# Kernel optimization log

Hardware: AMD Instinct MI355X
Metric: run time of the kernel (lower is better)

Reference implementation:

```python
import jax, jax.numpy as jnp
import numpy as np

EPS = 1e-8  # F.cosine_similarity eps


def _cosine(nb, q):
    # nb: [N1, k, d], q: [N1, d] -> [N1, k]
    dot = jnp.einsum('nkd,nd->nk', nb, q)
    nb_norm = jnp.maximum(jnp.linalg.norm(nb, axis=-1), EPS)
    q_norm = jnp.maximum(jnp.linalg.norm(q, axis=-1), EPS)[:, None]
    return dot / (nb_norm * q_norm)


def setup_inputs() -> dict:
    key = jax.random.key(0)
    k0, k1, k2, k3 = jax.random.split(key, 4)
    N1, N2, D = 2048, 50000, 512
    return {
        'query_emb0': jax.random.normal(k0, (N1, D), dtype=jnp.float32),
        'query_emb1': jax.random.normal(k1, (N1, D), dtype=jnp.float32),
        'cand_emb0': jax.random.normal(k2, (N2, D), dtype=jnp.float32),
        'cand_emb1': jax.random.normal(k3, (N2, D), dtype=jnp.float32),
        'k': 32,
    }


def reference(query_emb0, query_emb1, cand_emb0, cand_emb1, k):
    # --- get_KNN_batch: L2 cdist on the ORIGINAL embeddings only (matches torch) ---
    # ||q - c||^2 = ||q||^2 + ||c||^2 - 2 q.c  (GEMM-based, compute-bound)
    q2 = jnp.sum(query_emb0 * query_emb0, axis=1, keepdims=True)       # [N1,1]
    c2 = jnp.sum(cand_emb0 * cand_emb0, axis=1)[None, :]               # [1,N2]
    d2 = jnp.maximum(q2 + c2 - 2.0 * (query_emb0 @ cand_emb0.T), 0.0)  # [N1,N2]
    dist = jnp.sqrt(d2)
    # topk of -distance == k nearest
    _, top_k_idx = jax.lax.top_k(-dist, k)                             # [N1,k]

    # --- get_neighbor_embeddings: gather both tables ---
    nb0 = cand_emb0[top_k_idx]  # [N1,k,d]
    nb1 = cand_emb1[top_k_idx]  # [N1,k,d]

    # --- compute_cosine_batch: elementwise max of the two cosine tables ---
    cos0 = _cosine(nb0, query_emb0)
    cos1 = _cosine(nb1, query_emb1)
    cosine_table = jnp.where(cos0 > cos1, cos0, cos1)                  # [N1,k]
    return cosine_table, jnp.mean(cosine_table, axis=-1)
```

## Files before the change

kernel.cpp:

```cpp
#include <hip/hip_runtime.h>
#include <math.h>


#define D       512
#define KSEL    32
#define NSELMX  64
#define NCF     8
#define TOPL    5
#define CEPS    1e-8f
#define INF     __builtin_inff()

#define MTF     32
#define NTF     256
#define KCF     64
#define NTHF    256

#define MT      64
#define NT      512
#define KC      64
#define NTH     512

using s16x8  = __attribute__((ext_vector_type(8)))  short;
using f32x16 = __attribute__((ext_vector_type(16))) float;

__device__ __forceinline__ void async16(const void* g, void* s) {
  __builtin_amdgcn_global_load_lds(
      (const __attribute__((address_space(1))) unsigned int*)g,
      (__attribute__((address_space(3))) unsigned int*)s, 16, 0, 0);
}

__device__ __forceinline__ unsigned int bfhi2(float x0, float x1) {
  unsigned int u0 = __float_as_uint(x0), u1 = __float_as_uint(x1);
  u0 = (u0 + 0x7fffu + ((u0 >> 16) & 1u)) >> 16;
  u1 = (u1 + 0x7fffu + ((u1 >> 16) & 1u)) & 0xffff0000u;
  return u0 | u1;
}

__global__ __launch_bounds__(256) void sumsq_cvt_kernel(
    const float* __restrict__ C, const float* __restrict__ Q,
    float* __restrict__ c2, float* __restrict__ q2,
    unsigned short* __restrict__ Cb, unsigned short* __restrict__ Qb,
    int n2, int n1)
{
  int wid  = threadIdx.x >> 6;
  int lane = threadIdx.x & 63;
  int row  = blockIdx.x * 4 + wid;
  const float* src; float* dst; unsigned short* bdst;
  if (row < n2) { src = C + (size_t)row * D; dst = c2 + row; bdst = Cb + (size_t)row * D; }
  else {
    int r = row - n2; if (r >= n1) return;
    src = Q + (size_t)r * D; dst = q2 + r; bdst = Qb + (size_t)r * D;
  }
  const float4* s4 = (const float4*)src;
  float4 a = s4[2*lane], b = s4[2*lane + 1];
  float s = a.x*a.x + a.y*a.y + a.z*a.z + a.w*a.w
          + b.x*b.x + b.y*b.y + b.z*b.z + b.w*b.w;
  int4 h;
  h.x = (int)bfhi2(a.x, a.y); h.y = (int)bfhi2(a.z, a.w);
  h.z = (int)bfhi2(b.x, b.y); h.w = (int)bfhi2(b.z, b.w);
  *(int4*)(bdst + 8*lane) = h;
  #pragma unroll
  for (int o = 32; o > 0; o >>= 1) s += __shfl_down(s, o, 64);
  if (lane == 0) *dst = s;
}

__global__ __launch_bounds__(256) void rows_sumsq_kernel(
    const float* __restrict__ C, const float* __restrict__ Q,
    float* __restrict__ c2, float* __restrict__ q2, int n2, int n1)
{
  int wid  = threadIdx.x >> 6;
  int lane = threadIdx.x & 63;
  int row  = blockIdx.x * 4 + wid;
  const float* src; float* dst;
  if (row < n2) { src = C + (size_t)row * D; dst = c2 + row; }
  else { int r = row - n2; if (r >= n1) return; src = Q + (size_t)r * D; dst = q2 + r; }
  const float4* s4 = (const float4*)src;
  float4 a = s4[lane], b = s4[lane + 64];
  float s = a.x*a.x + a.y*a.y + a.z*a.z + a.w*a.w
          + b.x*b.x + b.y*b.y + b.z*b.z + b.w*b.w;
  #pragma unroll
  for (int o = 32; o > 0; o >>= 1) s += __shfl_down(s, o, 64);
  if (lane == 0) *dst = s;
}

__device__ inline void worst_reduce(float dIn, int iIn, float& wd, int& wi) {
  float dd = dIn; int ii = iIn;
  #pragma unroll
  for (int o = 1; o <= 16; o <<= 1) {
    float dp = __shfl_xor(dd, o, 64);
    int   ip = __shfl_xor(ii, o, 64);
    bool take = (dp > dd) || (dp == dd && ip > ii);
    dd = take ? dp : dd; ii = take ? ip : ii;
  }
  wd = __shfl(dd, 0, 64); wi = __shfl(ii, 0, 64);
}

__device__ inline void cvt8(const float4 a, const float4 b, int4& hi, int4& lo) {
  float x[8] = {a.x, a.y, a.z, a.w, b.x, b.y, b.z, b.w};
  unsigned int hw[8], lw[8];
  #pragma unroll
  for (int j = 0; j < 8; ++j) {
    unsigned int ux = __float_as_uint(x[j]);
    unsigned int rh = (ux + 0x7fffu + ((ux >> 16) & 1u)) & 0xffff0000u;
    float rl = x[j] - __uint_as_float(rh);
    unsigned int ul = __float_as_uint(rl);
    hw[j] = rh >> 16;
    lw[j] = (ul + 0x7fffu + ((ul >> 16) & 1u)) >> 16;
  }
  hi = make_int4((int)(hw[0]|(hw[1]<<16)), (int)(hw[2]|(hw[3]<<16)),
                 (int)(hw[4]|(hw[5]<<16)), (int)(hw[6]|(hw[7]<<16)));
  lo = make_int4((int)(lw[0]|(lw[1]<<16)), (int)(lw[2]|(lw[3]<<16)),
                 (int)(lw[4]|(lw[5]<<16)), (int)(lw[6]|(lw[7]<<16)));
}

__global__ __launch_bounds__(NTHF, 2) void knn_phase1_bf_kernel(
    const unsigned short* __restrict__ Qb, const unsigned short* __restrict__ Cb,
    const float* __restrict__ q2g, const float* __restrict__ c2g,
    float* __restrict__ tkd, int* __restrict__ tki,
    int n1, int n2, int chunk, int nc)
{
  extern __shared__ char smem[];
  unsigned short* qh = (unsigned short*)smem;
  unsigned short* ch = (unsigned short*)(smem + 8192);
  float* dl = (float*)(smem + 73728);

  const int tid  = threadIdx.x;
  const int w    = tid >> 6;
  const int l    = tid & 63;
  const int l31  = l & 31;
  const int half = l >> 5;
  const int bid     = blockIdx.x;
  const int chunkid = bid & (NCF - 1);
  const int mbase   = (bid >> 3) * MTF;
  const int cbase0  = chunkid * chunk;
  const int cend    = min(cbase0 + chunk, n2);

  float q2w[8];
  #pragma unroll
  for (int g = 0; g < 8; ++g)
    q2w[g] = q2g[min(mbase + 8*(g>>1) + 2*w + (g&1), n1 - 1)];

  unsigned long long vv[8][TOPL];
  #pragma unroll
  for (int g = 0; g < 8; ++g)
    #pragma unroll
    for (int t = 0; t < TOPL; ++t) vv[g][t] = 0xffffffffffffffffULL;

  const int lrow = l >> 3;
  const int su   = (l & 7) ^ lrow;

  auto STAGE = [&](int buf, int kb, int cb) {
    {
      int gm = min(mbase + w*8 + lrow, n1 - 1);
      const unsigned short* src = Qb + (size_t)gm * D + kb*KCF + su*8;
      unsigned short* dst = qh + buf*(32*64) + (w*8)*64;
      async16(src, dst);
    }
    #pragma unroll
    for (int i = 0; i < 8; ++i) {
      int gn = cb + w*64 + i*8 + lrow;
      const unsigned short* src = Cb + (size_t)gn * D + kb*KCF + su*8;
      unsigned short* dst = ch + buf*(256*64) + (w*64 + i*8)*64;
      async16(src, dst);
    }
  };

  f32x16 zf;
  #pragma unroll
  for (int e = 0; e < 16; ++e) zf[e] = 0.f;

  const int nsteps = (cend - cbase0 + NTF - 1) / NTF;
  int b = 0;
  STAGE(0, 0, cbase0);
  __syncthreads();

  for (int nt = 0; nt < nsteps; ++nt) {
    const int cbase = cbase0 + nt * NTF;
    f32x16 acc[2];
    acc[0] = zf; acc[1] = zf;

    for (int kb = 0; kb < D/KCF; ++kb) {
      if (kb + 1 < D/KCF) {
        STAGE(b^1, kb+1, cbase);
        asm volatile("s_waitcnt vmcnt(9)" ::: "memory");
      } else if (nt + 1 < nsteps) {
        STAGE(b^1, 0, cbase + NTF);
        asm volatile("s_waitcnt vmcnt(9)" ::: "memory");
      } else {
        asm volatile("s_waitcnt vmcnt(0)" ::: "memory");
      }
      __builtin_amdgcn_s_barrier();
      __builtin_amdgcn_sched_barrier(0);

      const unsigned short* qb  = qh + b*(32*64);
      const unsigned short* cbf = ch + b*(256*64);
      #pragma unroll
      for (int ks = 0; ks < 4; ++ks) {
        const int u = 2*ks + half;
        s16x8 qf, cf[2];
        {
          int r = l31;
          qf = *(const s16x8*)(qb + r*64 + (u ^ (r & 7))*8);
        }
        #pragma unroll
        for (int ct = 0; ct < 2; ++ct) {
          int c = w*64 + ct*32 + l31;
          cf[ct] = *(const s16x8*)(cbf + c*64 + (u ^ (c & 7))*8);
        }
        #pragma unroll
        for (int ct = 0; ct < 2; ++ct)
          acc[ct] = __builtin_amdgcn_mfma_f32_32x32x16_bf16(qf, cf[ct], acc[ct], 0, 0, 0);
      }
      asm volatile("s_waitcnt lgkmcnt(0)" ::: "memory");
      __builtin_amdgcn_s_barrier();
      __builtin_amdgcn_sched_barrier(0);
      b ^= 1;
    }

    float c2v[2]; int vld[2];
    #pragma unroll
    for (int ct = 0; ct < 2; ++ct) {
      int gc = cbase + w*64 + ct*32 + l31;
      vld[ct] = (gc < cend);
      c2v[ct] = vld[ct] ? c2g[gc] : 0.f;
    }
    #pragma unroll
    for (int p = 0; p < 4; ++p) {
      #pragma unroll
      for (int jj = 0; jj < 4; ++jj)
        #pragma unroll
        for (int ct = 0; ct < 2; ++ct) {
          float a = acc[ct][4*p + jj];
          float s = c2v[ct] - 2.f * a;
          dl[(4*half + jj)*NTF + w*64 + ct*32 + l31] = vld[ct] ? s : INF;
        }
      __syncthreads();
      #pragma unroll
      for (int s2 = 0; s2 < 2; ++s2) {
        const int g = 2*p + s2;
        const float q2u = q2w[g];
        #pragma unroll
        for (int j2 = 0; j2 < 4; ++j2) {
          float sv  = dl[(2*w + s2)*NTF + l + 64*j2];
          float d2v = fmaxf(q2u + sv, 0.f);
          unsigned int kbit = __float_as_uint(d2v);
          unsigned int ci = (kbit != 0x7f800000u) ? (unsigned)(cbase + 64*j2 + l)
                                                  : 0x7fffffffu;
          unsigned long long e = ((unsigned long long)kbit << 32) | ci;
          if (e < vv[g][TOPL-1]) {
            vv[g][TOPL-1] = e;
            #pragma unroll
            for (int t = TOPL-1; t > 0; --t) {
              unsigned long long lo = vv[g][t-1] < vv[g][t] ? vv[g][t-1] : vv[g][t];
              unsigned long long hi = vv[g][t-1] < vv[g][t] ? vv[g][t]   : vv[g][t-1];
              vv[g][t-1] = lo; vv[g][t] = hi;
            }
          }
        }
      }
      __syncthreads();
    }
  }

  unsigned long long* sel = (unsigned long long*)smem + (size_t)w * 2048;
  const unsigned long long mlt = (l == 0) ? 0ull : ((~0ull) >> (64 - l));
  __syncthreads();
  #pragma unroll
  for (int g = 0; g < 8; ++g) {
    unsigned int pk = (unsigned int)(vv[g][0] >> 32);
    #pragma unroll
    for (int o = 1; o < 64; o <<= 1) {
      unsigned int other = (unsigned int)__shfl_xor((int)pk, o, 64);
      pk = (other > pk) ? other : pk;
    }
    int cnt = 0;
    #pragma unroll
    for (int t = 0; t < TOPL; ++t) cnt += ((unsigned int)(vv[g][t] >> 32) <= pk) ? 1 : 0;
    unsigned long long b0 = __ballot(cnt & 1);
    unsigned long long b1 = __ballot(cnt & 2);
    unsigned long long b2 = __ballot(cnt & 4);
    int pre = __popcll(b0 & mlt) + 2*__popcll(b1 & mlt) + 4*__popcll(b2 & mlt);
    int Ns  = __popcll(b0) + 2*__popcll(b1) + 4*__popcll(b2);
    #pragma unroll
    for (int t = 0; t < TOPL; ++t)
      if (t < cnt) sel[pre + t] = vv[g][t];
    asm volatile("s_waitcnt lgkmcnt(0)" ::: "memory");
    __builtin_amdgcn_sched_barrier(0);
    int rk[TOPL];
    #pragma unroll
    for (int t = 0; t < TOPL; ++t) rk[t] = 0;
    for (int j = 0; j < Ns; ++j) {
      unsigned long long e = sel[j];
      #pragma unroll
      for (int t = 0; t < TOPL; ++t) rk[t] += (e < vv[g][t]) ? 1 : 0;
    }
    int gq = mbase + 8*(g>>1) + 2*w + (g&1);
    if (gq < n1) {
      #pragma unroll
      for (int t = 0; t < TOPL; ++t)
        if (t < cnt && rk[t] < KSEL) {
          size_t o = ((size_t)gq * nc + chunkid) * KSEL + rk[t];
          tkd[o] = __uint_as_float((unsigned int)(vv[g][t] >> 32));
          tki[o] = (int)(unsigned int)(vv[g][t] & 0xffffffffu);
        }
    }
  }
}

__global__ __launch_bounds__(NTH) void knn_phase1_cvt_kernel(
    const float* __restrict__ Q, const float* __restrict__ C,
    const float* __restrict__ q2g, const float* __restrict__ c2g,
    float* __restrict__ tkd, int* __restrict__ tki,
    int n1, int n2, int chunk, int nc)
{
  extern __shared__ char smem[];
  unsigned short* qh = (unsigned short*)smem;
  unsigned short* ql = qh + 64*64;
  unsigned short* ch = ql + 64*64;
  unsigned short* cl = ch + 512*64;
  float* dl = (float*)(smem + 147456);

  const int tid  = threadIdx.x;
  const int w    = tid >> 6;
  const int l    = tid & 63;
  const int l31  = l & 31;
  const int half = l >> 5;
  const int mbase   = blockIdx.x * MT;
  const int chunkid = blockIdx.y;
  const int cbase0  = chunkid * chunk;
  const int cend    = min(cbase0 + chunk, n2);

  float q2w[8];
  #pragma unroll
  for (int g = 0; g < 8; ++g) q2w[g] = q2g[min(mbase + g*8 + w, n1 - 1)];

  float listd[8]; int listi[8]; float wd4[8]; int wi4[8];
  #pragma unroll
  for (int g = 0; g < 8; ++g) { listd[g]=INF; listi[g]=0x7fffffff; wd4[g]=INF; wi4[g]=0x7fffffff; }

  const int srow = tid >> 3;
  const int sk8  = (tid & 7) * 8;
  const int su   = (tid & 7);

  float4 cva[8][2], qva[2];
  auto LOADR = [&](int kb, int cb) {
    {
      int gr = min(mbase + srow, n1 - 1);
      const float4* p = (const float4*)(Q + (size_t)gr * D + kb*KC + sk8);
      qva[0] = p[0]; qva[1] = p[1];
    }
    #pragma unroll
    for (int r = 0; r < 8; ++r) {
      int gn = cb + srow + 64*r;
      if (gn < cend) {
        const float4* p = (const float4*)(C + (size_t)gn * D + kb*KC + sk8);
        cva[r][0] = p[0]; cva[r][1] = p[1];
      } else {
        cva[r][0] = make_float4(0.f,0.f,0.f,0.f);
        cva[r][1] = make_float4(0.f,0.f,0.f,0.f);
      }
    }
  };
  auto STORE = [&]() {
    int4 hi, lo;
    {
      int idx = srow*64 + (su ^ (srow & 7))*8;
      cvt8(qva[0], qva[1], hi, lo);
      *(int4*)(qh + idx) = hi; *(int4*)(ql + idx) = lo;
    }
    #pragma unroll
    for (int r = 0; r < 8; ++r) {
      int row = srow + 64*r;
      int idx = row*64 + (su ^ (row & 7))*8;
      cvt8(cva[r][0], cva[r][1], hi, lo);
      *(int4*)(ch + idx) = hi; *(int4*)(cl + idx) = lo;
    }
  };

  f32x16 zf;
  #pragma unroll
  for (int e = 0; e < 16; ++e) zf[e] = 0.f;

  const int nsteps = (cend - cbase0 + NT - 1) / NT;
  LOADR(0, cbase0);

  for (int nt = 0; nt < nsteps; ++nt) {
    const int cbase = cbase0 + nt * NT;
    f32x16 acc[2][2];
    #pragma unroll
    for (int rt = 0; rt < 2; ++rt)
      #pragma unroll
      for (int ct = 0; ct < 2; ++ct) acc[rt][ct] = zf;

    for (int kb = 0; kb < D/KC; ++kb) {
      __syncthreads();
      STORE();
      __syncthreads();
      if (kb + 1 < D/KC)        LOADR(kb + 1, cbase);
      else if (nt + 1 < nsteps) LOADR(0, cbase + NT);

      #pragma unroll
      for (int ks = 0; ks < 4; ++ks) {
        const int u = 2*ks + half;
        s16x8 qf[2][2], cf[2][2];
        #pragma unroll
        for (int rt = 0; rt < 2; ++rt) {
          int r = rt*32 + l31;
          int idx = r*64 + (u ^ (r & 7))*8;
          qf[rt][0] = *(const s16x8*)(qh + idx);
          qf[rt][1] = *(const s16x8*)(ql + idx);
        }
        #pragma unroll
        for (int ct = 0; ct < 2; ++ct) {
          int c = w*64 + ct*32 + l31;
          int idx = c*64 + (u ^ (c & 7))*8;
          cf[ct][0] = *(const s16x8*)(ch + idx);
          cf[ct][1] = *(const s16x8*)(cl + idx);
        }
        #pragma unroll
        for (int rt = 0; rt < 2; ++rt)
          #pragma unroll
          for (int ct = 0; ct < 2; ++ct) {
            acc[rt][ct] = __builtin_amdgcn_mfma_f32_32x32x16_bf16(qf[rt][0], cf[ct][0], acc[rt][ct], 0, 0, 0);
            acc[rt][ct] = __builtin_amdgcn_mfma_f32_32x32x16_bf16(qf[rt][0], cf[ct][1], acc[rt][ct], 0, 0, 0);
            acc[rt][ct] = __builtin_amdgcn_mfma_f32_32x32x16_bf16(qf[rt][1], cf[ct][0], acc[rt][ct], 0, 0, 0);
          }
      }
    }

    float c2v[2]; int vld[2];
    #pragma unroll
    for (int ct = 0; ct < 2; ++ct) {
      int gc = cbase + w*64 + ct*32 + l31;
      vld[ct] = (gc < cend);
      c2v[ct] = vld[ct] ? c2g[gc] : 0.f;
    }
    #pragma unroll
    for (int g = 0; g < 8; ++g) {
      const int rt = g >> 2, qq = g & 3;
      #pragma unroll
      for (int jj = 0; jj < 4; ++jj)
        #pragma unroll
        for (int ct = 0; ct < 2; ++ct) {
          float a = acc[rt][ct][4*qq + jj];
          float s = c2v[ct] - 2.f * a;
          dl[(4*half + jj)*512 + w*64 + ct*32 + l31] = vld[ct] ? s : INF;
        }
      __syncthreads();
      const float q2u = q2w[g];
      #pragma unroll
      for (int j2 = 0; j2 < 8; ++j2) {
        float sv = dl[w*512 + l + 64*j2];
        float dv = sqrtf(fmaxf(q2u + sv, 0.f));
        unsigned long long mask = __ballot(dv < wd4[g]);
        while (mask) {
          int L = __ffsll(mask) - 1; mask &= mask - 1;
          float dnew = __shfl(dv, L, 64);
          int ci = cbase + 64*j2 + L;
          if ((dnew < wd4[g]) || (dnew == wd4[g] && ci < wi4[g])) {
            bool isw = (l < 32) && (listd[g] == wd4[g]) && (listi[g] == wi4[g]);
            int wl = __ffsll(__ballot(isw)) - 1;
            if (l == wl) { listd[g] = dnew; listi[g] = ci; }
            worst_reduce((l < 32) ? listd[g] : -1.f,
                         (l < 32) ? listi[g] : -1, wd4[g], wi4[g]);
          }
        }
      }
      __syncthreads();
    }
  }

  #pragma unroll
  for (int g = 0; g < 8; ++g) {
    int gq = mbase + g*8 + w;
    float d = listd[g]; int i = listi[g];
    int rank = 0;
    #pragma unroll
    for (int j = 0; j < KSEL; ++j) {
      float dj = __shfl(listd[g], j, 64);
      int   ij = __shfl(listi[g], j, 64);
      rank += (dj < d) || (dj == d && ij < i);
    }
    if (l < 32 && gq < n1) {
      size_t o = ((size_t)gq * nc + chunkid) * KSEL + rank;
      tkd[o] = d; tki[o] = i;
    }
  }
}

__global__ __launch_bounds__(256) void knn_phase2_kernel(
    const float* __restrict__ Q0, const float* __restrict__ Q1,
    const float* __restrict__ C0, const float* __restrict__ C1,
    const float* __restrict__ q2g, const float* __restrict__ c2g,
    const float* __restrict__ tkd, const int* __restrict__ tki,
    float* __restrict__ out, int n1, int n2, int nc)
{
  __shared__ float q0s[D], q1s[D];
  __shared__ float pd[256]; __shared__ int pi[256];
  __shared__ float nd[NSELMX]; __shared__ int ni[NSELMX];
  __shared__ float de[NSELMX];
  __shared__ int   fi[KSEL];
  __shared__ float cosj[KSEL];
  __shared__ float red0[4], red1[4], qn[2];

  const int q = blockIdx.x, tid = threadIdx.x;
  const int npool = nc * KSEL;
  const int nsel  = (NSELMX < npool) ? NSELMX : npool;

  if (tid < 128) ((float4*)q0s)[tid] = ((const float4*)(Q0 + (size_t)q*D))[tid];
  else           ((float4*)q1s)[tid-128] = ((const float4*)(Q1 + (size_t)q*D))[tid-128];
  if (tid < npool) { pd[tid] = tkd[(size_t)q*npool + tid]; pi[tid] = tki[(size_t)q*npool + tid]; }
  __syncthreads();

  float a0 = q0s[tid], b0 = q0s[tid+256], a1 = q1s[tid], b1 = q1s[tid+256];
  float s0 = a0*a0 + b0*b0, s1 = a1*a1 + b1*b1;
  #pragma unroll
  for (int o = 32; o > 0; o >>= 1) { s0 += __shfl_down(s0, o, 64); s1 += __shfl_down(s1, o, 64); }
  int lane = tid & 63, wid = tid >> 6;
  if (lane == 0) { red0[wid] = s0; red1[wid] = s1; }

  if (tid < npool) {
    float dm = pd[tid]; int im = pi[tid]; int rank = 0;
    for (int j = 0; j < npool; ++j) {
      float dj = pd[j]; int ij = pi[j];
      rank += (dj < dm) || (dj == dm && ij < im);
    }
    if (rank < nsel) { nd[rank] = dm; ni[rank] = im; }
  }
  __syncthreads();
  if (tid == 0) {
    qn[0] = fmaxf(sqrtf(red0[0]+red0[1]+red0[2]+red0[3]), CEPS);
    qn[1] = fmaxf(sqrtf(red1[0]+red1[1]+red1[2]+red1[3]), CEPS);
  }

  const float q2q = q2g[q];
  const int ll = tid & 7;
  for (int base = 0; base < NSELMX; base += 32) {
    int g = base + (tid >> 3);
    if (g < nsel) {
      int ix = ni[g];
      bool okx = (ix >= 0 && ix < n2);
      int ixc = okx ? ix : 0;
      const float4* r0  = (const float4*)(C0 + (size_t)ixc * D);
      const float4* q04 = (const float4*)q0s;
      float dot = 0.f;
      #pragma unroll
      for (int r = 0; r < 16; ++r) {
        float4 v = r0[r*8 + ll], u = q04[r*8 + ll];
        dot = fmaf(v.x,u.x, fmaf(v.y,u.y, fmaf(v.z,u.z, fmaf(v.w,u.w, dot))));
      }
      #pragma unroll
      for (int o = 4; o > 0; o >>= 1) dot += __shfl_xor(dot, o, 64);
      if (ll == 0) de[g] = okx ? sqrtf(fmaxf(q2q + c2g[ixc] - 2.f*dot, 0.f)) : INF;
    }
  }
  __syncthreads();

  if (tid < nsel) {
    float dm = de[tid]; int im = ni[tid]; int rank = 0;
    for (int j = 0; j < nsel; ++j) {
      float dj = de[j]; int ij = ni[j];
      rank += (dj < dm) || (dj == dm && ij < im);
    }
    if (rank < KSEL) fi[rank] = im;
  }
  __syncthreads();

  const int g = tid >> 3;
  int ix = fi[g];
  ix = (ix >= 0 && ix < n2) ? ix : 0;
  const float4* r0  = (const float4*)(C0 + (size_t)ix * D);
  const float4* r1  = (const float4*)(C1 + (size_t)ix * D);
  const float4* q04 = (const float4*)q0s;
  const float4* q14 = (const float4*)q1s;
  float dot0 = 0.f, nn0 = 0.f, dot1 = 0.f, nn1 = 0.f;
  #pragma unroll
  for (int r = 0; r < 16; ++r) {
    int e4 = r*8 + ll;
    float4 v0 = r0[e4], qv0 = q04[e4];
    dot0 = fmaf(v0.x,qv0.x, fmaf(v0.y,qv0.y, fmaf(v0.z,qv0.z, fmaf(v0.w,qv0.w, dot0))));
    nn0  = fmaf(v0.x,v0.x,  fmaf(v0.y,v0.y,  fmaf(v0.z,v0.z,  fmaf(v0.w,v0.w,  nn0))));
    float4 v1 = r1[e4], qv1 = q14[e4];
    dot1 = fmaf(v1.x,qv1.x, fmaf(v1.y,qv1.y, fmaf(v1.z,qv1.z, fmaf(v1.w,qv1.w, dot1))));
    nn1  = fmaf(v1.x,v1.x,  fmaf(v1.y,v1.y,  fmaf(v1.z,v1.z,  fmaf(v1.w,v1.w,  nn1))));
  }
  #pragma unroll
  for (int o = 4; o > 0; o >>= 1) {
    dot0 += __shfl_xor(dot0, o, 64); nn0 += __shfl_xor(nn0, o, 64);
    dot1 += __shfl_xor(dot1, o, 64); nn1 += __shfl_xor(nn1, o, 64);
  }
  if (ll == 0) {
    float c0 = dot0 / (fmaxf(sqrtf(nn0), CEPS) * qn[0]);
    float c1 = dot1 / (fmaxf(sqrtf(nn1), CEPS) * qn[1]);
    float cv = (c0 > c1) ? c0 : c1;
    out[(size_t)q * KSEL + g] = cv;
    cosj[g] = cv;
  }
  __syncthreads();
  if (tid == 0) {
    float s = 0.f;
    #pragma unroll
    for (int j = 0; j < KSEL; ++j) s += cosj[j];
    out[(size_t)n1 * KSEL + q] = s * (1.f / KSEL);
  }
}

extern "C" void kernel_launch(void* const* d_in, const int* in_sizes, int n_in,
                              void* d_out, int out_size, void* d_ws, size_t ws_size,
                              hipStream_t stream)
{
  const float* Q0 = (const float*)d_in[0];
  const float* Q1 = (const float*)d_in[1];
  const float* C0 = (const float*)d_in[2];
  const float* C1 = (const float*)d_in[3];
  const int n1 = in_sizes[0] / D;
  const int n2 = in_sizes[2] / D;
  float* out = (float*)d_out;
  if (n1 <= 0 || n2 <= 0) return;

  char* wsb = (char*)d_ws;
  size_t c2n = ((size_t)n2 + 127) & ~(size_t)127;
  size_t q2n = ((size_t)n1 + 127) & ~(size_t)127;

  size_t off_c2  = 0;
  size_t off_q2  = off_c2 + c2n*4;
  size_t off_tkd = off_q2 + q2n*4;
  size_t off_tki = off_tkd + (size_t)n1*NCF*KSEL*4;
  size_t off_cb  = (off_tki + (size_t)n1*NCF*KSEL*4 + 255) & ~(size_t)255;
  size_t off_qb  = off_cb + ((size_t)n2 + 512)*D*2;
  size_t need    = off_qb + (size_t)n1*D*2;
  bool fast = (ws_size >= need);

  if (fast) {
    float* c2  = (float*)(wsb + off_c2);
    float* q2  = (float*)(wsb + off_q2);
    float* tkd = (float*)(wsb + off_tkd);
    int*   tki = (int*)(wsb + off_tki);
    unsigned short* Cb = (unsigned short*)(wsb + off_cb);
    unsigned short* Qb = (unsigned short*)(wsb + off_qb);

    sumsq_cvt_kernel<<<(n2 + n1 + 3)/4, 256, 0, stream>>>(C0, Q0, c2, q2, Cb, Qb, n2, n1);

    const int chunk  = (n2 + NCF - 1) / NCF;
    const int mtiles = (n1 + MTF - 1) / MTF;
    (void)hipFuncSetAttribute((const void*)knn_phase1_bf_kernel,
                              hipFuncAttributeMaxDynamicSharedMemorySize, 81920);
    knn_phase1_bf_kernel<<<mtiles * NCF, NTHF, 81920, stream>>>(
        Qb, Cb, q2, c2, tkd, tki, n1, n2, chunk, NCF);
    knn_phase2_kernel<<<n1, 256, 0, stream>>>(Q0, Q1, C0, C1, q2, c2, tkd, tki, out, n1, n2, NCF);
  } else {
    float* wsf = (float*)d_ws;
    int nc = 8;
    while (nc > 1 && (c2n + q2n + (size_t)n1 * nc * KSEL * 2) * 4 > ws_size) nc >>= 1;
    float* c2  = wsf;
    float* q2  = wsf + c2n;
    float* tkd = wsf + c2n + q2n;
    int*   tki = (int*)(wsf + c2n + q2n + (size_t)n1 * nc * KSEL);

    rows_sumsq_kernel<<<(n2 + n1 + 3)/4, 256, 0, stream>>>(C0, Q0, c2, q2, n2, n1);
    const int chunk  = (n2 + nc - 1) / nc;
    const int mtiles = (n1 + MT - 1) / MT;
    (void)hipFuncSetAttribute((const void*)knn_phase1_cvt_kernel,
                              hipFuncAttributeMaxDynamicSharedMemorySize, 163840);
    knn_phase1_cvt_kernel<<<dim3(mtiles, nc), NTH, 163840, stream>>>(
        Q0, C0, q2, c2, tkd, tki, n1, n2, chunk, nc);
    knn_phase2_kernel<<<n1, 256, 0, stream>>>(Q0, Q1, C0, C1, q2, c2, tkd, tki, out, n1, n2, nc);
  }
}
```

Measured before the change: 479.7 us.

## Keep query tile in registers and vectorize top-k distance reads

The whole 32-row query tile (all of D for each lane's row) is loaded once into registers (128 VGPRs of bf16 fragments) rather than staged through shared memory each k-step. This removes one async copy per stage and the per-step LDS query reads, and cuts shared memory from 80 KB to 72 KB. The top-k scan now reads four consecutive distances with one float4 load, with candidate indices changed to match. The risks are higher register pressure and spilling under launch_bounds(256,2), plus possible LDS bank conflicts from the strided float4 reads.

```diff
diff --git a/kernel.cpp b/kernel.cpp
--- a/kernel.cpp
+++ b/kernel.cpp
@@ -120,9 +120,8 @@
     int n1, int n2, int chunk, int nc)
 {
   extern __shared__ char smem[];
-  unsigned short* qh = (unsigned short*)smem;
-  unsigned short* ch = (unsigned short*)(smem + 8192);
-  float* dl = (float*)(smem + 73728);
+  unsigned short* ch = (unsigned short*)smem;
+  float* dl = (float*)(smem + 65536);
 
   const int tid  = threadIdx.x;
   const int w    = tid >> 6;
@@ -140,6 +139,17 @@
   for (int g = 0; g < 8; ++g)
     q2w[g] = q2g[min(mbase + 8*(g>>1) + 2*w + (g&1), n1 - 1)];
 
+  s16x8 qreg[8][4];
+  {
+    int gm = min(mbase + l31, n1 - 1);
+    const unsigned short* qrow = Qb + (size_t)gm * D + half*8;
+    #pragma unroll
+    for (int kb = 0; kb < 8; ++kb)
+      #pragma unroll
+      for (int ks = 0; ks < 4; ++ks)
+        qreg[kb][ks] = *(const s16x8*)(qrow + kb*64 + ks*16);
+  }
+
   unsigned long long vv[8][TOPL];
   #pragma unroll
   for (int g = 0; g < 8; ++g)
@@ -150,12 +160,6 @@
   const int su   = (l & 7) ^ lrow;
 
   auto STAGE = [&](int buf, int kb, int cb) {
-    {
-      int gm = min(mbase + w*8 + lrow, n1 - 1);
-      const unsigned short* src = Qb + (size_t)gm * D + kb*KCF + su*8;
-      unsigned short* dst = qh + buf*(32*64) + (w*8)*64;
-      async16(src, dst);
-    }
     #pragma unroll
     for (int i = 0; i < 8; ++i) {
       int gn = cb + w*64 + i*8 + lrow;
@@ -179,37 +183,32 @@
     f32x16 acc[2];
     acc[0] = zf; acc[1] = zf;
 
-    for (int kb = 0; kb < D/KCF; ++kb) {
-      if (kb + 1 < D/KCF) {
+    #pragma unroll
+    for (int kb = 0; kb < 8; ++kb) {
+      if (kb + 1 < 8) {
         STAGE(b^1, kb+1, cbase);
-        asm volatile("s_waitcnt vmcnt(9)" ::: "memory");
+        asm volatile("s_waitcnt vmcnt(8)" ::: "memory");
       } else if (nt + 1 < nsteps) {
         STAGE(b^1, 0, cbase + NTF);
-        asm volatile("s_waitcnt vmcnt(9)" ::: "memory");
+        asm volatile("s_waitcnt vmcnt(8)" ::: "memory");
       } else {
         asm volatile("s_waitcnt vmcnt(0)" ::: "memory");
       }
       __builtin_amdgcn_s_barrier();
       __builtin_amdgcn_sched_barrier(0);
 
-      const unsigned short* qb  = qh + b*(32*64);
       const unsigned short* cbf = ch + b*(256*64);
       #pragma unroll
       for (int ks = 0; ks < 4; ++ks) {
         const int u = 2*ks + half;
-        s16x8 qf, cf[2];
-        {
-          int r = l31;
-          qf = *(const s16x8*)(qb + r*64 + (u ^ (r & 7))*8);
-        }
+        s16x8 cf[2];
         #pragma unroll
         for (int ct = 0; ct < 2; ++ct) {
           int c = w*64 + ct*32 + l31;
           cf[ct] = *(const s16x8*)(cbf + c*64 + (u ^ (c & 7))*8);
         }
-        #pragma unroll
-        for (int ct = 0; ct < 2; ++ct)
-          acc[ct] = __builtin_amdgcn_mfma_f32_32x32x16_bf16(qf, cf[ct], acc[ct], 0, 0, 0);
+        acc[0] = __builtin_amdgcn_mfma_f32_32x32x16_bf16(qreg[kb][ks], cf[0], acc[0], 0, 0, 0);
+        acc[1] = __builtin_amdgcn_mfma_f32_32x32x16_bf16(qreg[kb][ks], cf[1], acc[1], 0, 0, 0);
       }
       asm volatile("s_waitcnt lgkmcnt(0)" ::: "memory");
       __builtin_amdgcn_s_barrier();
@@ -239,12 +238,13 @@
       for (int s2 = 0; s2 < 2; ++s2) {
         const int g = 2*p + s2;
         const float q2u = q2w[g];
+        float4 sv4 = *((const float4*)(dl + (2*w + s2)*NTF) + l);
+        float svs[4] = {sv4.x, sv4.y, sv4.z, sv4.w};
         #pragma unroll
-        for (int j2 = 0; j2 < 4; ++j2) {
-          float sv  = dl[(2*w + s2)*NTF + l + 64*j2];
-          float d2v = fmaxf(q2u + sv, 0.f);
+        for (int jj = 0; jj < 4; ++jj) {
+          float d2v = fmaxf(q2u + svs[jj], 0.f);
           unsigned int kbit = __float_as_uint(d2v);
-          unsigned int ci = (kbit != 0x7f800000u) ? (unsigned)(cbase + 64*j2 + l)
+          unsigned int ci = (kbit != 0x7f800000u) ? (unsigned)(cbase + 4*l + jj)
                                                   : 0x7fffffffu;
           unsigned long long e = ((unsigned long long)kbit << 32) | ci;
           if (e < vv[g][TOPL-1]) {
@@ -644,8 +644,8 @@
     const int chunk  = (n2 + NCF - 1) / NCF;
     const int mtiles = (n1 + MTF - 1) / MTF;
     (void)hipFuncSetAttribute((const void*)knn_phase1_bf_kernel,
-                              hipFuncAttributeMaxDynamicSharedMemorySize, 81920);
-    knn_phase1_bf_kernel<<<mtiles * NCF, NTHF, 81920, stream>>>(
+                              hipFuncAttributeMaxDynamicSharedMemorySize, 73728);
+    knn_phase1_bf_kernel<<<mtiles * NCF, NTHF, 73728, stream>>>(
         Qb, Cb, q2, c2, tkd, tki, n1, n2, chunk, NCF);
     knn_phase2_kernel<<<n1, 256, 0, stream>>>(Q0, Q1, C0, C1, q2, c2, tkd, tki, out, n1, n2, NCF);
   } else {
```

Measured after the change: 492.8 us. 2.7% more time.
